# Kernel optimization log

Hardware: AMD Instinct MI355X
Metric: run time of the kernel (lower is better)

The kernel has to match this reference:

```python
import jax, jax.numpy as jnp
import numpy as np

B, T, IMG, P, D, H, L = 4, 32, 84, 14, 768, 12, 3
GP = IMG // P            # 6 patches per side
NP = GP * GP             # 36 patches
N = NP + 1               # +cls token
FF = 4 * D
HD = D // H


def _ln(x, g, b):
    m = jnp.mean(x, -1, keepdims=True)
    v = jnp.var(x, -1, keepdims=True)
    return (x - m) * jax.lax.rsqrt(v + 1e-5) * g + b


def _mha(x, qkv_w, qkv_b, proj_w, proj_b):
    Bn, Nn, C = x.shape
    qkv = (x @ qkv_w + qkv_b).reshape(Bn, Nn, 3, H, HD).transpose(2, 0, 3, 1, 4)
    q, k, v = qkv[0], qkv[1], qkv[2]                      # (B,H,N,hd)
    attn = jax.nn.softmax(jnp.einsum('bhqd,bhkd->bhqk', q, k) * HD ** -0.5, axis=-1)
    o = jnp.einsum('bhqk,bhkd->bhqd', attn, v).transpose(0, 2, 1, 3).reshape(Bn, Nn, C)
    return o @ proj_w + proj_b


def _blocks(x, pre_g, pre_b, n1_g, n1_b, qkv_w, qkv_b, proj_w, proj_b,
            n2_g, n2_b, fc1_w, fc1_b, fc2_w, fc2_b):
    # TemporalViT applies an extra pre-norm, then x = x + Block(x_norm),
    # where Block itself contains two residual sublayers on x_norm.
    for i in range(L):
        xn = _ln(x, pre_g[i], pre_b[i])
        y = xn + _mha(_ln(xn, n1_g[i], n1_b[i]), qkv_w[i], qkv_b[i], proj_w[i], proj_b[i])
        h = jax.nn.gelu(_ln(y, n2_g[i], n2_b[i]) @ fc1_w[i] + fc1_b[i], approximate=False)
        y = y + h @ fc2_w[i] + fc2_b[i]
        x = x + y
    return x


def _forward(x, conv_w, conv_b, cls, pos, tpos,
             s_pre_g, s_pre_b, s_n1_g, s_n1_b, s_qkv_w, s_qkv_b, s_proj_w, s_proj_b,
             s_n2_g, s_n2_b, s_fc1_w, s_fc1_b, s_fc2_w, s_fc2_b,
             t_pre_g, t_pre_b, t_n1_g, t_n1_b, t_qkv_w, t_qkv_b, t_proj_w, t_proj_b,
             t_n2_g, t_n2_b, t_fc1_w, t_fc1_b, t_fc2_w, t_fc2_b):
    xf = x.reshape(B * T, 3, IMG, IMG)
    p = jax.lax.conv_general_dilated(xf, conv_w, (P, P), 'VALID',
                                     dimension_numbers=('NCHW', 'OIHW', 'NCHW'))
    p = p + conv_b[None, :, None, None]                  # (BT, D, 6, 6)
    p = p.reshape(B * T, D, NP).transpose(0, 2, 1)       # (BT, 36, D)
    p = jnp.concatenate([jnp.broadcast_to(cls, (B * T, 1, D)), p], axis=1) + pos
    p = _blocks(p, s_pre_g, s_pre_b, s_n1_g, s_n1_b, s_qkv_w, s_qkv_b, s_proj_w,
                s_proj_b, s_n2_g, s_n2_b, s_fc1_w, s_fc1_b, s_fc2_w, s_fc2_b)
    p = p.reshape(B, T * N, D)
    tp = jnp.broadcast_to(tpos[:, :T, None, :], (1, T, N, D)).reshape(1, T * N, D)
    p = p + tp
    p = _blocks(p, t_pre_g, t_pre_b, t_n1_g, t_n1_b, t_qkv_w, t_qkv_b, t_proj_w,
                t_proj_b, t_n2_g, t_n2_b, t_fc1_w, t_fc1_b, t_fc2_w, t_fc2_b)
    return p.mean(axis=1)                                # (B, D)


def setup_inputs() -> dict:
    key = jax.random.key(0)
    ks = iter(jax.random.split(key, 64))
    r = lambda shape, s=0.02: (jax.random.normal(next(ks), shape, jnp.float32) * s)
    inp = {
        'x': jax.random.normal(next(ks), (B, T, 3, IMG, IMG), jnp.float32),
        'conv_w': r((D, 3, P, P)), 'conv_b': jnp.zeros((D,), jnp.float32),
        'cls': r((1, 1, D)), 'pos': r((1, N, D)), 'tpos': r((1, 100, D)),
    }
    for pfx in ('s', 't'):
        inp[f'{pfx}_pre_g'] = jnp.ones((L, D), jnp.float32)
        inp[f'{pfx}_pre_b'] = jnp.zeros((L, D), jnp.float32)
        inp[f'{pfx}_n1_g'] = jnp.ones((L, D), jnp.float32)
        inp[f'{pfx}_n1_b'] = jnp.zeros((L, D), jnp.float32)
        inp[f'{pfx}_qkv_w'] = r((L, D, 3 * D))
        inp[f'{pfx}_qkv_b'] = jnp.zeros((L, 3 * D), jnp.float32)
        inp[f'{pfx}_proj_w'] = r((L, D, D))
        inp[f'{pfx}_proj_b'] = jnp.zeros((L, D), jnp.float32)
        inp[f'{pfx}_n2_g'] = jnp.ones((L, D), jnp.float32)
        inp[f'{pfx}_n2_b'] = jnp.zeros((L, D), jnp.float32)
        inp[f'{pfx}_fc1_w'] = r((L, D, FF))
        inp[f'{pfx}_fc1_b'] = jnp.zeros((L, FF), jnp.float32)
        inp[f'{pfx}_fc2_w'] = r((L, FF, D))
        inp[f'{pfx}_fc2_b'] = jnp.zeros((L, D), jnp.float32)
    return inp


def reference(x, conv_w, conv_b, cls, pos, tpos,
              s_pre_g, s_pre_b, s_n1_g, s_n1_b, s_qkv_w, s_qkv_b, s_proj_w, s_proj_b,
              s_n2_g, s_n2_b, s_fc1_w, s_fc1_b, s_fc2_w, s_fc2_b,
              t_pre_g, t_pre_b, t_n1_g, t_n1_b, t_qkv_w, t_qkv_b, t_proj_w, t_proj_b,
              t_n2_g, t_n2_b, t_fc1_w, t_fc1_b, t_fc2_w, t_fc2_b):
    return _forward(x, conv_w, conv_b, cls, pos, tpos,
                    s_pre_g, s_pre_b, s_n1_g, s_n1_b, s_qkv_w, s_qkv_b, s_proj_w,
                    s_proj_b, s_n2_g, s_n2_b, s_fc1_w, s_fc1_b, s_fc2_w, s_fc2_b,
                    t_pre_g, t_pre_b, t_n1_g, t_n1_b, t_qkv_w, t_qkv_b, t_proj_w,
                    t_proj_b, t_n2_g, t_n2_b, t_fc1_w, t_fc1_b, t_fc2_w, t_fc2_b)
```

## Files before the change

### kernel.cpp

```cpp
#include <hip/hip_runtime.h>
#include <math.h>

#define NTOK 4736
#define MPAD 4864
#define DM   768
#define NHEAD 12
#define KC   640

typedef __attribute__((ext_vector_type(8))) short bf16x8;
typedef __attribute__((ext_vector_type(4))) float f32x4;

__device__ inline short f2bf(float f) {
  union { float f; unsigned u; } v; v.f = f;
  unsigned r = v.u + 0x7FFF + ((v.u >> 16) & 1);
  return (short)(r >> 16);
}

__device__ inline void gload16(const void* g, void* l) {
  __builtin_amdgcn_global_load_lds(
      (const __attribute__((address_space(1))) void*)g,
      (__attribute__((address_space(3))) void*)l, 16, 0, 0);
}

__global__ __launch_bounds__(256) void im2col_k(const float* __restrict__ x,
                                                short* __restrict__ col) {
  int i = blockIdx.x * 256 + threadIdx.x;
  int r = i / KC, k = i % KC;
  short v = 0;
  if (k < 588) {
    int bt = r / 36, p = r % 36;
    int gy = p / 6, gx = p % 6;
    int c = k / 196, rem = k % 196;
    int ky = rem / 14, kx = rem % 14;
    v = f2bf(x[(((size_t)bt * 3 + c) * 84 + gy * 14 + ky) * 84 + gx * 14 + kx]);
  }
  col[i] = v;
}

__global__ __launch_bounds__(256) void convw_k(const float* __restrict__ w,
                                               short* __restrict__ out) {
  int i = blockIdx.x * 256 + threadIdx.x;
  int n = i / KC, k = i % KC;
  out[i] = (k < 588) ? f2bf(w[(size_t)n * 588 + k]) : (short)0;
}

__global__ __launch_bounds__(256) void wt_k(const float* __restrict__ in,
                                            short* __restrict__ out,
                                            int K, int N) {
  __shared__ float tile[32][33];
  const int l = blockIdx.z;
  in  += (size_t)l * K * N;
  out += (size_t)l * N * K;
  const int n0 = blockIdx.x * 32, k0 = blockIdx.y * 32;
  const int tx = threadIdx.x & 31, ty = threadIdx.x >> 5;
#pragma unroll
  for (int r = 0; r < 4; r++)
    tile[ty + 8 * r][tx] = in[(size_t)(k0 + ty + 8 * r) * N + n0 + tx];
  __syncthreads();
#pragma unroll
  for (int r = 0; r < 4; r++)
    out[(size_t)(n0 + ty + 8 * r) * K + k0 + tx] = f2bf(tile[tx][ty + 8 * r]);
}

__global__ __launch_bounds__(256) void assemble_k(const float* __restrict__ conv_out,
                                                  const float* __restrict__ cls,
                                                  const float* __restrict__ pos,
                                                  float* __restrict__ X) {
  int i = blockIdx.x * 256 + threadIdx.x;
  int t = i / DM, d = i % DM;
  int bt = t / 37, n = t % 37;
  float v = (n == 0) ? cls[d] : conv_out[((size_t)bt * 36 + (n - 1)) * DM + d];
  X[i] = v + pos[n * DM + d];
}

__global__ __launch_bounds__(256) void tpos_k(float* __restrict__ X,
                                              const float* __restrict__ tpos) {
  int i = blockIdx.x * 256 + threadIdx.x;
  int row = i / DM, d = i % DM;
  int tt = (row % 1184) / 37;
  X[i] += tpos[tt * DM + d];
}

template <bool OBF>
__global__ __launch_bounds__(256) void ln_k(const float* __restrict__ in,
                                            const float* __restrict__ g,
                                            const float* __restrict__ b,
                                            void* __restrict__ outp) {
  int r = blockIdx.x;
  int tid = threadIdx.x;
  const float* xr = in + (size_t)r * DM;
  float v0 = xr[tid], v1 = xr[tid + 256], v2 = xr[tid + 512];
  float s  = v0 + v1 + v2;
  float sq = v0 * v0 + v1 * v1 + v2 * v2;
#pragma unroll
  for (int off = 32; off; off >>= 1) {
    s  += __shfl_down(s, off);
    sq += __shfl_down(sq, off);
  }
  __shared__ float ss[4], sg[4];
  if ((tid & 63) == 0) { ss[tid >> 6] = s; sg[tid >> 6] = sq; }
  __syncthreads();
  float S = ss[0] + ss[1] + ss[2] + ss[3];
  float Q = sg[0] + sg[1] + sg[2] + sg[3];
  float mean = S * (1.f / 768.f);
  float var  = Q * (1.f / 768.f) - mean * mean;
  float rs = rsqrtf(var + 1e-5f);
  float o0 = (v0 - mean) * rs * g[tid]       + b[tid];
  float o1 = (v1 - mean) * rs * g[tid + 256] + b[tid + 256];
  float o2 = (v2 - mean) * rs * g[tid + 512] + b[tid + 512];
  if (OBF) {
    short* o = (short*)outp + (size_t)r * DM;
    o[tid] = f2bf(o0); o[tid + 256] = f2bf(o1); o[tid + 512] = f2bf(o2);
  } else {
    float* o = (float*)outp + (size_t)r * DM;
    o[tid] = o0; o[tid + 256] = o1; o[tid + 512] = o2;
  }
}

__global__ __launch_bounds__(256) void ln2_k(const float* __restrict__ in,
                                             const float* __restrict__ g1,
                                             const float* __restrict__ b1,
                                             const float* __restrict__ g2,
                                             const float* __restrict__ b2,
                                             float* __restrict__ xn,
                                             short* __restrict__ w) {
  int r = blockIdx.x;
  int tid = threadIdx.x;
  const float* xr = in + (size_t)r * DM;
  float v0 = xr[tid], v1 = xr[tid + 256], v2 = xr[tid + 512];
  float s  = v0 + v1 + v2;
  float sq = v0 * v0 + v1 * v1 + v2 * v2;
#pragma unroll
  for (int off = 32; off; off >>= 1) {
    s  += __shfl_down(s, off);
    sq += __shfl_down(sq, off);
  }
  __shared__ float ss[4], sg[4], ss2[4], sg2[4];
  if ((tid & 63) == 0) { ss[tid >> 6] = s; sg[tid >> 6] = sq; }
  __syncthreads();
  float S = ss[0] + ss[1] + ss[2] + ss[3];
  float Q = sg[0] + sg[1] + sg[2] + sg[3];
  float mean = S * (1.f / 768.f);
  float var  = Q * (1.f / 768.f) - mean * mean;
  float rs = rsqrtf(var + 1e-5f);
  float x0 = (v0 - mean) * rs * g1[tid]       + b1[tid];
  float x1 = (v1 - mean) * rs * g1[tid + 256] + b1[tid + 256];
  float x2 = (v2 - mean) * rs * g1[tid + 512] + b1[tid + 512];
  float* xo = xn + (size_t)r * DM;
  xo[tid] = x0; xo[tid + 256] = x1; xo[tid + 512] = x2;
  float s2  = x0 + x1 + x2;
  float sq2 = x0 * x0 + x1 * x1 + x2 * x2;
#pragma unroll
  for (int off = 32; off; off >>= 1) {
    s2  += __shfl_down(s2, off);
    sq2 += __shfl_down(sq2, off);
  }
  if ((tid & 63) == 0) { ss2[tid >> 6] = s2; sg2[tid >> 6] = sq2; }
  __syncthreads();
  float S2 = ss2[0] + ss2[1] + ss2[2] + ss2[3];
  float Q2 = sg2[0] + sg2[1] + sg2[2] + sg2[3];
  float mean2 = S2 * (1.f / 768.f);
  float var2  = Q2 * (1.f / 768.f) - mean2 * mean2;
  float rs2 = rsqrtf(var2 + 1e-5f);
  short* wo = w + (size_t)r * DM;
  wo[tid]       = f2bf((x0 - mean2) * rs2 * g2[tid]       + b2[tid]);
  wo[tid + 256] = f2bf((x1 - mean2) * rs2 * g2[tid + 256] + b2[tid + 256]);
  wo[tid + 512] = f2bf((x2 - mean2) * rs2 * g2[tid + 512] + b2[tid + 512]);
}

template <int BM, int BN, int WM, int WN, bool GELU, bool OBF, bool HASR1, bool HASR2>
__global__ __launch_bounds__(256, 2) void tgemm_k(const short* __restrict__ A,
                                                  const short* __restrict__ Bw,
                                                  const float* __restrict__ bias,
                                                  const float* __restrict__ r1,
                                                  const float* __restrict__ r2,
                                                  void* __restrict__ Cout,
                                                  int M, int N, int K) {
  constexpr int TM = BM / WM, TN = BN / WN;
  constexpr int MF = TM / 16, NF = TN / 16;
  constexpr int RPC = 32;
  constexpr int ACH = BM / RPC, BCH = BN / RPC;
  constexpr int LOADS = ACH + BCH;

  __shared__ short As[2][BM][64];
  __shared__ short Bs[2][BN][64];

  const int nwg  = gridDim.x * gridDim.y;
  const int orig = blockIdx.x + gridDim.x * blockIdx.y;
  const int qq = nwg >> 3, rr = nwg & 7;
  const int xcd = orig & 7, sub = orig >> 3;
  const int wgid = ((xcd < rr) ? xcd * (qq + 1) : rr * (qq + 1) + (xcd - rr) * qq) + sub;
  const int gy = gridDim.y;
  const int bm = (wgid / gy) * BM, bn = (wgid % gy) * BN;

  const int tid = threadIdx.x, wid = tid >> 6, lane = tid & 63;
  const int lr = lane & 15, lg = lane >> 4;
  const int wm = wid / WN, wn = wid % WN;

  const int srow = tid >> 3;
  const int sslot = (tid & 7) ^ (srow & 7);
  const short* Asrc = A  + (size_t)(bm + srow) * K + sslot * 8;
  const short* Bsrc = Bw + (size_t)(bn + srow) * K + sslot * 8;

  f32x4 acc[MF][NF];
#pragma unroll
  for (int m = 0; m < MF; m++)
#pragma unroll
    for (int n = 0; n < NF; n++) acc[m][n] = (f32x4){0.f, 0.f, 0.f, 0.f};

#define STAGE(slot, kk)                                                        \
  do {                                                                         \
    _Pragma("unroll")                                                          \
    for (int j = 0; j < ACH; j++)                                              \
      gload16(Asrc + (size_t)(j * RPC) * K + (kk),                             \
              (char*)&As[slot][0][0] + j * RPC * 128 + wid * 1024);            \
    _Pragma("unroll")                                                          \
    for (int j = 0; j < BCH; j++)                                              \
      gload16(Bsrc + (size_t)(j * RPC) * K + (kk),                             \
              (char*)&Bs[slot][0][0] + j * RPC * 128 + wid * 1024);            \
  } while (0)

  const int NT = K >> 6;
  const int swz = (lr & 7) << 4;

  STAGE(0, 0);
  for (int t = 0; t < NT; t++) {
    const int c = t & 1;
    if (t + 1 < NT) STAGE(c ^ 1, (t + 1) << 6);
    if (t + 1 < NT) {
      if constexpr (LOADS == 8)      asm volatile("s_waitcnt vmcnt(8)" ::: "memory");
      else if constexpr (LOADS == 6) asm volatile("s_waitcnt vmcnt(6)" ::: "memory");
      else                           asm volatile("s_waitcnt vmcnt(0)" ::: "memory");
    } else {
      asm volatile("s_waitcnt vmcnt(0)" ::: "memory");
    }
    __builtin_amdgcn_s_barrier();

    bf16x8 bq[NF][2], aq[MF][2];
#pragma unroll
    for (int nf = 0; nf < NF; nf++) {
      const int row = wn * TN + nf * 16 + lr;
#pragma unroll
      for (int ks = 0; ks < 2; ks++)
        bq[nf][ks] = *reinterpret_cast<const bf16x8*>(
            (const char*)&Bs[c][0][0] + row * 128 + ((ks * 64 + lg * 16) ^ swz));
    }
#pragma unroll
    for (int mf = 0; mf < MF; mf++) {
      const int row = wm * TM + mf * 16 + lr;
#pragma unroll
      for (int ks = 0; ks < 2; ks++)
        aq[mf][ks] = *reinterpret_cast<const bf16x8*>(
            (const char*)&As[c][0][0] + row * 128 + ((ks * 64 + lg * 16) ^ swz));
    }
    __builtin_amdgcn_s_setprio(1);
#pragma unroll
    for (int mf = 0; mf < MF; mf++)
#pragma unroll
      for (int nf = 0; nf < NF; nf++) {
        acc[mf][nf] = __builtin_amdgcn_mfma_f32_16x16x32_bf16(
            aq[mf][0], bq[nf][0], acc[mf][nf], 0, 0, 0);
        acc[mf][nf] = __builtin_amdgcn_mfma_f32_16x16x32_bf16(
            aq[mf][1], bq[nf][1], acc[mf][nf], 0, 0, 0);
      }
    __builtin_amdgcn_s_setprio(0);
    __builtin_amdgcn_s_barrier();
  }
#undef STAGE

#pragma unroll
  for (int m = 0; m < MF; m++) {
#pragma unroll
    for (int r = 0; r < 4; r++) {
      int row = bm + wm * TM + m * 16 + lg * 4 + r;
      if (row < M) {
#pragma unroll
        for (int n = 0; n < NF; n++) {
          int col = bn + wn * TN + n * 16 + lr;
          size_t idx = (size_t)row * N + col;
          float v = acc[m][n][r];
          if (bias) v += bias[col];
          if (GELU) v = 0.5f * v * (1.f + erff(v * 0.70710678118654752f));
          if (HASR1) v += r1[idx];
          if (HASR2) v += r2[idx];
          if (OBF) ((short*)Cout)[idx] = f2bf(v);
          else     ((float*)Cout)[idx] = v;
        }
      }
    }
  }
}

__global__ __launch_bounds__(256) void attn_k(const short* __restrict__ qkv,
                                              short* __restrict__ out,
                                              int Bn, int Nn) {
  const int gx = gridDim.x, gy = gridDim.y;
  const int nwg = gx * gy;
  const int orig = blockIdx.x + gx * blockIdx.y;
  const int qq = nwg >> 3, rr = nwg & 7;
  const int xcd = orig & 7, sub = orig >> 3;
  const int wgid = ((xcd < rr) ? xcd * (qq + 1) : rr * (qq + 1) + (xcd - rr) * qq) + sub;
  const int bh = wgid / gy;
  const int qb = wgid % gy;
  const int b = bh / NHEAD, h = bh % NHEAD;
  const int q0 = qb * 64;

  const int tid = threadIdx.x;
  const int wid = tid >> 6, lane = tid & 63;
  const int lr = lane & 15, lg = lane >> 4;

  __shared__ short Ks[64][64];
  __shared__ short Vt[64][64];
  __shared__ short Ps[4][16][64];

  const int qrow_in = q0 + wid * 16 + lr;
  const int qcl = (qrow_in < Nn) ? qrow_in : (Nn - 1);
  const short* qp = qkv + ((size_t)(b * Nn + qcl)) * 2304 + h * 64 + lg * 8;
  bf16x8 qa0 = *reinterpret_cast<const bf16x8*>(qp);
  bf16x8 qa1 = *reinterpret_cast<const bf16x8*>(qp + 32);

  f32x4 oo[4];
#pragma unroll
  for (int dg = 0; dg < 4; dg++) oo[dg] = (f32x4){0.f, 0.f, 0.f, 0.f};
  float mm[4] = {-1e30f, -1e30f, -1e30f, -1e30f};
  float ll[4] = {0.f, 0.f, 0.f, 0.f};

  const int skey = tid >> 2;
  const int sdq  = (tid & 3) * 16;
  const int vkey = tid & 63;
  const int vd0  = wid * 16;

  const int swr = (lr & 7) << 3;

  for (int k0 = 0; k0 < Nn; k0 += 64) {
    {
      int kg = k0 + skey; if (kg >= Nn) kg = Nn - 1;
      const short* kp = qkv + ((size_t)(b * Nn + kg)) * 2304 + 768 + h * 64 + sdq;
      bf16x8 ka = *reinterpret_cast<const bf16x8*>(kp);
      bf16x8 kb = *reinterpret_cast<const bf16x8*>(kp + 8);
      const int ksw = (skey & 7) << 3;
      *reinterpret_cast<bf16x8*>(&Ks[skey][sdq ^ ksw])       = ka;
      *reinterpret_cast<bf16x8*>(&Ks[skey][(sdq + 8) ^ ksw]) = kb;
      int vg = k0 + vkey; if (vg >= Nn) vg = Nn - 1;
      const short* vp = qkv + ((size_t)(b * Nn + vg)) * 2304 + 1536 + h * 64 + vd0;
      bf16x8 va = *reinterpret_cast<const bf16x8*>(vp);
      bf16x8 vb = *reinterpret_cast<const bf16x8*>(vp + 8);
#pragma unroll
      for (int i = 0; i < 8; i++) {
        Vt[vd0 + i][vkey ^ (i << 3)]     = va[i];
        Vt[vd0 + 8 + i][vkey ^ (i << 3)] = vb[i];
      }
    }
    __syncthreads();

    f32x4 c[4];
#pragma unroll
    for (int kf = 0; kf < 4; kf++) {
      c[kf] = (f32x4){0.f, 0.f, 0.f, 0.f};
      const short* krow = &Ks[kf * 16 + lr][0];
      bf16x8 kb0 = *reinterpret_cast<const bf16x8*>(krow + ((lg * 8) ^ swr));
      c[kf] = __builtin_amdgcn_mfma_f32_16x16x32_bf16(qa0, kb0, c[kf], 0, 0, 0);
      bf16x8 kb1 = *reinterpret_cast<const bf16x8*>(krow + ((32 + lg * 8) ^ swr));
      c[kf] = __builtin_amdgcn_mfma_f32_16x16x32_bf16(qa1, kb1, c[kf], 0, 0, 0);
    }
#pragma unroll
    for (int kf = 0; kf < 4; kf++) {
#pragma unroll
      for (int r = 0; r < 4; r++) c[kf][r] *= 0.125f;
      if (k0 + kf * 16 + lr >= Nn)
        c[kf][0] = c[kf][1] = c[kf][2] = c[kf][3] = -1e30f;
    }

#pragma unroll
    for (int r = 0; r < 4; r++) {
      float t = fmaxf(fmaxf(c[0][r], c[1][r]), fmaxf(c[2][r], c[3][r]));
      t = fmaxf(t, __shfl_xor(t, 1, 16));
      t = fmaxf(t, __shfl_xor(t, 2, 16));
      t = fmaxf(t, __shfl_xor(t, 4, 16));
      t = fmaxf(t, __shfl_xor(t, 8, 16));
      float mn = fmaxf(mm[r], t);
      float sc = __expf(mm[r] - mn);
      float p0 = __expf(c[0][r] - mn);
      float p1 = __expf(c[1][r] - mn);
      float p2 = __expf(c[2][r] - mn);
      float p3 = __expf(c[3][r] - mn);
      float ps = (p0 + p1) + (p2 + p3);
      ps += __shfl_xor(ps, 1, 16);
      ps += __shfl_xor(ps, 2, 16);
      ps += __shfl_xor(ps, 4, 16);
      ps += __shfl_xor(ps, 8, 16);
      ll[r] = ll[r] * sc + ps;
      mm[r] = mn;
      oo[0][r] *= sc; oo[1][r] *= sc; oo[2][r] *= sc; oo[3][r] *= sc;
      const int prow = lg * 4 + r;
      const int psw  = (prow & 7) << 3;
      short* pr = &Ps[wid][prow][0];
      pr[lr ^ psw]        = f2bf(p0);
      pr[(16 + lr) ^ psw] = f2bf(p1);
      pr[(32 + lr) ^ psw] = f2bf(p2);
      pr[(48 + lr) ^ psw] = f2bf(p3);
    }

#pragma unroll
    for (int ks = 0; ks < 2; ks++) {
      bf16x8 pa = *reinterpret_cast<const bf16x8*>(&Ps[wid][lr][(ks * 32 + lg * 8) ^ swr]);
#pragma unroll
      for (int dg = 0; dg < 4; dg++) {
        bf16x8 vb = *reinterpret_cast<const bf16x8*>(
            &Vt[dg * 16 + lr][(ks * 32 + lg * 8) ^ swr]);
        oo[dg] = __builtin_amdgcn_mfma_f32_16x16x32_bf16(pa, vb, oo[dg], 0, 0, 0);
      }
    }
    __syncthreads();
  }

#pragma unroll
  for (int r = 0; r < 4; r++) {
    int qr = q0 + wid * 16 + lg * 4 + r;
    if (qr < Nn) {
      float inv = 1.f / ll[r];
      short* op = out + ((size_t)(b * Nn + qr)) * DM + h * 64 + lr;
      op[0]  = f2bf(oo[0][r] * inv);
      op[16] = f2bf(oo[1][r] * inv);
      op[32] = f2bf(oo[2][r] * inv);
      op[48] = f2bf(oo[3][r] * inv);
    }
  }
}

__global__ __launch_bounds__(256) void mean1_k(const float* __restrict__ X,
                                               float* __restrict__ P) {
  int b = blockIdx.x, seg = blockIdx.z;
  int d = blockIdx.y * 256 + threadIdx.x;
  int r0 = seg * 148;
  float s = 0.f;
  for (int r = r0; r < r0 + 148; r++) s += X[((size_t)b * 1184 + r) * DM + d];
  P[((size_t)(b * 8 + seg)) * DM + d] = s;
}
__global__ __launch_bounds__(256) void mean2_k(const float* __restrict__ P,
                                               float* __restrict__ out) {
  int b = blockIdx.x;
  int d = blockIdx.y * 256 + threadIdx.x;
  float s = 0.f;
#pragma unroll
  for (int seg = 0; seg < 8; seg++) s += P[((size_t)(b * 8 + seg)) * DM + d];
  out[b * DM + d] = s * (1.f / 1184.f);
}

extern "C" void kernel_launch(void* const* d_in, const int* in_sizes, int n_in,
                              void* d_out, int out_size, void* d_ws, size_t ws_size,
                              hipStream_t stream) {
  (void)in_sizes; (void)n_in; (void)out_size; (void)ws_size;
  const float* x      = (const float*)d_in[0];
  const float* conv_w = (const float*)d_in[1];
  const float* conv_b = (const float*)d_in[2];
  const float* cls    = (const float*)d_in[3];
  const float* pos    = (const float*)d_in[4];
  const float* tpos   = (const float*)d_in[5];
  const float* W[2][14];
  for (int p = 0; p < 2; p++)
    for (int i = 0; i < 14; i++)
      W[p][i] = (const float*)d_in[6 + p * 14 + i];

  char* ws = (char*)d_ws;
  const size_t TOKF = (size_t)NTOK * DM * 4;
  float* X    = (float*)(ws);
  float* XN   = (float*)(ws + TOKF);
  float* Y    = (float*)(ws + 2 * TOKF);
  short* TA2  = (short*)(ws + 3 * TOKF);
  short* BIG  = (short*)(ws + 3 * TOKF + (size_t)MPAD * DM * 2);
  short* WB   = (short*)(ws + 3 * TOKF + (size_t)MPAD * DM * 2
                            + (size_t)MPAD * 3072 * 2);
  const size_t QE = (size_t)3 * 2304 * 768;
  const size_t PE = (size_t)3 * 768 * 768;
  const size_t F1E = (size_t)3 * 3072 * 768;
  const size_t F2E = (size_t)3 * 768 * 3072;
  const size_t PFX = QE + PE + F1E + F2E;
  short* WQ[2], *WP[2], *WF1[2], *WF2[2];
  for (int p = 0; p < 2; p++) {
    WQ[p]  = WB + p * PFX;
    WP[p]  = WQ[p] + QE;
    WF1[p] = WP[p] + PE;
    WF2[p] = WF1[p] + F1E;
  }
  short* CW = WB + 2 * PFX;
  float* PB = (float*)(CW + (size_t)768 * KC);

  for (int p = 0; p < 2; p++) {
    wt_k<<<dim3(72, 24, 3), 256, 0, stream>>>(W[p][4],  WQ[p],  768, 2304);
    wt_k<<<dim3(24, 24, 3), 256, 0, stream>>>(W[p][6],  WP[p],  768, 768);
    wt_k<<<dim3(96, 24, 3), 256, 0, stream>>>(W[p][10], WF1[p], 768, 3072);
    wt_k<<<dim3(24, 96, 3), 256, 0, stream>>>(W[p][12], WF2[p], 3072, 768);
  }
  convw_k<<<1920, 256, 0, stream>>>(conv_w, CW);

  im2col_k<<<11520, 256, 0, stream>>>(x, BIG);
  tgemm_k<64, 128, 1, 4, false, false, false, false><<<dim3(72, 6), 256, 0, stream>>>(
      BIG, CW, conv_b, nullptr, nullptr, Y, 4608, 768, KC);
  assemble_k<<<14208, 256, 0, stream>>>(Y, cls, pos, X);

  for (int phase = 0; phase < 2; phase++) {
    const int Bn = (phase == 0) ? 128 : 4;
    const int Nn = (phase == 0) ? 37 : 1184;
    if (phase == 1) tpos_k<<<14208, 256, 0, stream>>>(X, tpos);
    for (int i = 0; i < 3; i++) {
      const float* pre_g = W[phase][0] + i * DM;
      const float* pre_b = W[phase][1] + i * DM;
      const float* n1_g  = W[phase][2] + i * DM;
      const float* n1_b  = W[phase][3] + i * DM;
      const float* qkv_b = W[phase][5] + i * 2304;
      const float* prj_b = W[phase][7] + i * DM;
      const float* n2_g  = W[phase][8] + i * DM;
      const float* n2_b  = W[phase][9] + i * DM;
      const float* fc1_b = W[phase][11] + i * 3072;
      const float* fc2_b = W[phase][13] + i * DM;
      const short* qkv_w = WQ[phase]  + (size_t)i * 2304 * 768;
      const short* prj_w = WP[phase]  + (size_t)i * 768 * 768;
      const short* fc1_w = WF1[phase] + (size_t)i * 3072 * 768;
      const short* fc2_w = WF2[phase] + (size_t)i * 768 * 3072;

      ln2_k<<<NTOK, 256, 0, stream>>>(X, pre_g, pre_b, n1_g, n1_b, XN, TA2);
      tgemm_k<128, 128, 2, 2, false, true, false, false><<<dim3(37, 18), 256, 0, stream>>>(
          TA2, qkv_w, qkv_b, nullptr, nullptr, BIG, NTOK, 2304, DM);
      attn_k<<<dim3(Bn * NHEAD, (Nn + 63) / 64), 256, 0, stream>>>(BIG, TA2, Bn, Nn);
      tgemm_k<64, 128, 1, 4, false, false, true, false><<<dim3(74, 6), 256, 0, stream>>>(
          TA2, prj_w, prj_b, XN, nullptr, Y, NTOK, DM, DM);
      ln_k<true><<<NTOK, 256, 0, stream>>>(Y, n2_g, n2_b, TA2);
      tgemm_k<128, 128, 2, 2, true, true, false, false><<<dim3(37, 24), 256, 0, stream>>>(
          TA2, fc1_w, fc1_b, nullptr, nullptr, BIG, NTOK, 3072, DM);
      tgemm_k<64, 128, 1, 4, false, false, true, true><<<dim3(74, 6), 256, 0, stream>>>(
          BIG, fc2_w, fc2_b, Y, X, X, NTOK, DM, 3072);
    }
  }
  mean1_k<<<dim3(4, 3, 8), 256, 0, stream>>>(X, PB);
  mean2_k<<<dim3(4, 3), 256, 0, stream>>>(PB, (float*)d_out);
}
```

Before: 1.612 ms.

## Replace LDS-staged GEMM with register-direct global-load MFMA GEMM

Replaces the double-buffered LDS-staged GEMM with a kernel in which each wave loads its A and B fragments straight from global memory into registers and feeds the MFMAs, with no shared memory or barriers. This is meant to remove LDS traffic and synchronisation overhead. In exchange there is no cross-wave reuse through LDS, so every wave refetches its operands from L2. The global reads are also strided 16-byte loads without software pipelining, and the padded-M buffers and the row bound check are dropped.

```diff
diff --git a/kernel.cpp b/kernel.cpp
--- a/kernel.cpp
+++ b/kernel.cpp
@@ -2,7 +2,6 @@
 #include <math.h>
 
 #define NTOK 4736
-#define MPAD 4864
 #define DM   768
 #define NHEAD 12
 #define KC   640
@@ -14,12 +13,6 @@
   union { float f; unsigned u; } v; v.f = f;
   unsigned r = v.u + 0x7FFF + ((v.u >> 16) & 1);
   return (short)(r >> 16);
-}
-
-__device__ inline void gload16(const void* g, void* l) {
-  __builtin_amdgcn_global_load_lds(
-      (const __attribute__((address_space(1))) void*)g,
-      (__attribute__((address_space(3))) void*)l, 16, 0, 0);
 }
 
 __global__ __launch_bounds__(256) void im2col_k(const float* __restrict__ x,
@@ -168,124 +161,76 @@
   wo[tid + 512] = f2bf((x2 - mean2) * rs2 * g2[tid + 512] + b2[tid + 512]);
 }
 
-template <int BM, int BN, int WM, int WN, bool GELU, bool OBF, bool HASR1, bool HASR2>
-__global__ __launch_bounds__(256, 2) void tgemm_k(const short* __restrict__ A,
-                                                  const short* __restrict__ Bw,
-                                                  const float* __restrict__ bias,
-                                                  const float* __restrict__ r1,
-                                                  const float* __restrict__ r2,
-                                                  void* __restrict__ Cout,
-                                                  int M, int N, int K) {
-  constexpr int TM = BM / WM, TN = BN / WN;
-  constexpr int MF = TM / 16, NF = TN / 16;
-  constexpr int RPC = 32;
-  constexpr int ACH = BM / RPC, BCH = BN / RPC;
-  constexpr int LOADS = ACH + BCH;
-
-  __shared__ short As[2][BM][64];
-  __shared__ short Bs[2][BN][64];
-
+template <int WM, int WN, bool GELU, bool OBF, bool HASR1, bool HASR2>
+__global__ __launch_bounds__(WM * WN * 64) void rgemm_k(const short* __restrict__ A,
+                                                        const short* __restrict__ Bw,
+                                                        const float* __restrict__ bias,
+                                                        const float* __restrict__ r1,
+                                                        const float* __restrict__ r2,
+                                                        void* __restrict__ Cout,
+                                                        int M, int N, int K) {
   const int nwg  = gridDim.x * gridDim.y;
   const int orig = blockIdx.x + gridDim.x * blockIdx.y;
   const int qq = nwg >> 3, rr = nwg & 7;
   const int xcd = orig & 7, sub = orig >> 3;
   const int wgid = ((xcd < rr) ? xcd * (qq + 1) : rr * (qq + 1) + (xcd - rr) * qq) + sub;
   const int gy = gridDim.y;
-  const int bm = (wgid / gy) * BM, bn = (wgid % gy) * BN;
+  const int bm = (wgid / gy) * (WM * 64), bn = (wgid % gy) * (WN * 64);
 
   const int tid = threadIdx.x, wid = tid >> 6, lane = tid & 63;
   const int lr = lane & 15, lg = lane >> 4;
   const int wm = wid / WN, wn = wid % WN;
 
-  const int srow = tid >> 3;
-  const int sslot = (tid & 7) ^ (srow & 7);
-  const short* Asrc = A  + (size_t)(bm + srow) * K + sslot * 8;
-  const short* Bsrc = Bw + (size_t)(bn + srow) * K + sslot * 8;
-
-  f32x4 acc[MF][NF];
-#pragma unroll
-  for (int m = 0; m < MF; m++)
-#pragma unroll
-    for (int n = 0; n < NF; n++) acc[m][n] = (f32x4){0.f, 0.f, 0.f, 0.f};
-
-#define STAGE(slot, kk)                                                        \
-  do {                                                                         \
-    _Pragma("unroll")                                                          \
-    for (int j = 0; j < ACH; j++)                                              \
-      gload16(Asrc + (size_t)(j * RPC) * K + (kk),                             \
-              (char*)&As[slot][0][0] + j * RPC * 128 + wid * 1024);            \
-    _Pragma("unroll")                                                          \
-    for (int j = 0; j < BCH; j++)                                              \
-      gload16(Bsrc + (size_t)(j * RPC) * K + (kk),                             \
-              (char*)&Bs[slot][0][0] + j * RPC * 128 + wid * 1024);            \
-  } while (0)
-
-  const int NT = K >> 6;
-  const int swz = (lr & 7) << 4;
-
-  STAGE(0, 0);
-  for (int t = 0; t < NT; t++) {
-    const int c = t & 1;
-    if (t + 1 < NT) STAGE(c ^ 1, (t + 1) << 6);
-    if (t + 1 < NT) {
-      if constexpr (LOADS == 8)      asm volatile("s_waitcnt vmcnt(8)" ::: "memory");
-      else if constexpr (LOADS == 6) asm volatile("s_waitcnt vmcnt(6)" ::: "memory");
-      else                           asm volatile("s_waitcnt vmcnt(0)" ::: "memory");
-    } else {
-      asm volatile("s_waitcnt vmcnt(0)" ::: "memory");
-    }
-    __builtin_amdgcn_s_barrier();
-
-    bf16x8 bq[NF][2], aq[MF][2];
-#pragma unroll
-    for (int nf = 0; nf < NF; nf++) {
-      const int row = wn * TN + nf * 16 + lr;
+  const short* Ap0 = A  + (size_t)(bm + wm * 64 + lr) * K + lg * 8;
+  const short* Bp0 = Bw + (size_t)(bn + wn * 64 + lr) * K + lg * 8;
+
+  f32x4 acc[4][4];
+#pragma unroll
+  for (int m = 0; m < 4; m++)
+#pragma unroll
+    for (int n = 0; n < 4; n++) acc[m][n] = (f32x4){0.f, 0.f, 0.f, 0.f};
+
+  for (int k0 = 0; k0 < K; k0 += 64) {
+    bf16x8 aq[4][2], bq[4][2];
+#pragma unroll
+    for (int mf = 0; mf < 4; mf++)
+#pragma unroll
+      for (int ks = 0; ks < 2; ks++)
+        aq[mf][ks] = *reinterpret_cast<const bf16x8*>(
+            Ap0 + (size_t)(mf * 16) * K + k0 + ks * 32);
+#pragma unroll
+    for (int nf = 0; nf < 4; nf++)
 #pragma unroll
       for (int ks = 0; ks < 2; ks++)
         bq[nf][ks] = *reinterpret_cast<const bf16x8*>(
-            (const char*)&Bs[c][0][0] + row * 128 + ((ks * 64 + lg * 16) ^ swz));
-    }
-#pragma unroll
-    for (int mf = 0; mf < MF; mf++) {
-      const int row = wm * TM + mf * 16 + lr;
-#pragma unroll
-      for (int ks = 0; ks < 2; ks++)
-        aq[mf][ks] = *reinterpret_cast<const bf16x8*>(
-            (const char*)&As[c][0][0] + row * 128 + ((ks * 64 + lg * 16) ^ swz));
-    }
-    __builtin_amdgcn_s_setprio(1);
-#pragma unroll
-    for (int mf = 0; mf < MF; mf++)
-#pragma unroll
-      for (int nf = 0; nf < NF; nf++) {
+            Bp0 + (size_t)(nf * 16) * K + k0 + ks * 32);
+#pragma unroll
+    for (int mf = 0; mf < 4; mf++)
+#pragma unroll
+      for (int nf = 0; nf < 4; nf++) {
         acc[mf][nf] = __builtin_amdgcn_mfma_f32_16x16x32_bf16(
             aq[mf][0], bq[nf][0], acc[mf][nf], 0, 0, 0);
         acc[mf][nf] = __builtin_amdgcn_mfma_f32_16x16x32_bf16(
             aq[mf][1], bq[nf][1], acc[mf][nf], 0, 0, 0);
       }
-    __builtin_amdgcn_s_setprio(0);
-    __builtin_amdgcn_s_barrier();
-  }
-#undef STAGE
-
-#pragma unroll
-  for (int m = 0; m < MF; m++) {
+  }
+
+#pragma unroll
+  for (int m = 0; m < 4; m++) {
 #pragma unroll
     for (int r = 0; r < 4; r++) {
-      int row = bm + wm * TM + m * 16 + lg * 4 + r;
-      if (row < M) {
-#pragma unroll
-        for (int n = 0; n < NF; n++) {
-          int col = bn + wn * TN + n * 16 + lr;
-          size_t idx = (size_t)row * N + col;
-          float v = acc[m][n][r];
-          if (bias) v += bias[col];
-          if (GELU) v = 0.5f * v * (1.f + erff(v * 0.70710678118654752f));
-          if (HASR1) v += r1[idx];
-          if (HASR2) v += r2[idx];
-          if (OBF) ((short*)Cout)[idx] = f2bf(v);
-          else     ((float*)Cout)[idx] = v;
-        }
+      int row = bm + wm * 64 + m * 16 + lg * 4 + r;
+#pragma unroll
+      for (int n = 0; n < 4; n++) {
+        int col = bn + wn * 64 + n * 16 + lr;
+        size_t idx = (size_t)row * N + col;
+        float v = acc[m][n][r];
+        if (bias) v += bias[col];
+        if (GELU) v = 0.5f * v * (1.f + erff(v * 0.70710678118654752f));
+        if (HASR1) v += r1[idx];
+        if (HASR2) v += r2[idx];
+        if (OBF) ((short*)Cout)[idx] = f2bf(v);
+        else     ((float*)Cout)[idx] = v;
       }
     }
   }
@@ -468,9 +413,9 @@
   float* XN   = (float*)(ws + TOKF);
   float* Y    = (float*)(ws + 2 * TOKF);
   short* TA2  = (short*)(ws + 3 * TOKF);
-  short* BIG  = (short*)(ws + 3 * TOKF + (size_t)MPAD * DM * 2);
-  short* WB   = (short*)(ws + 3 * TOKF + (size_t)MPAD * DM * 2
-                            + (size_t)MPAD * 3072 * 2);
+  short* BIG  = (short*)(ws + 3 * TOKF + (size_t)NTOK * DM * 2);
+  short* WB   = (short*)(ws + 3 * TOKF + (size_t)NTOK * DM * 2
+                            + (size_t)NTOK * 3072 * 2);
   const size_t QE = (size_t)3 * 2304 * 768;
   const size_t PE = (size_t)3 * 768 * 768;
   const size_t F1E = (size_t)3 * 3072 * 768;
@@ -495,7 +440,7 @@
   convw_k<<<1920, 256, 0, stream>>>(conv_w, CW);
 
   im2col_k<<<11520, 256, 0, stream>>>(x, BIG);
-  tgemm_k<64, 128, 1, 4, false, false, false, false><<<dim3(72, 6), 256, 0, stream>>>(
+  rgemm_k<2, 1, false, false, false, false><<<dim3(36, 12), 128, 0, stream>>>(
       BIG, CW, conv_b, nullptr, nullptr, Y, 4608, 768, KC);
   assemble_k<<<14208, 256, 0, stream>>>(Y, cls, pos, X);
 
@@ -520,15 +465,15 @@
       const short* fc2_w = WF2[phase] + (size_t)i * 768 * 3072;
 
       ln2_k<<<NTOK, 256, 0, stream>>>(X, pre_g, pre_b, n1_g, n1_b, XN, TA2);
-      tgemm_k<128, 128, 2, 2, false, true, false, false><<<dim3(37, 18), 256, 0, stream>>>(
+      rgemm_k<2, 2, false, true, false, false><<<dim3(37, 18), 256, 0, stream>>>(
           TA2, qkv_w, qkv_b, nullptr, nullptr, BIG, NTOK, 2304, DM);
       attn_k<<<dim3(Bn * NHEAD, (Nn + 63) / 64), 256, 0, stream>>>(BIG, TA2, Bn, Nn);
-      tgemm_k<64, 128, 1, 4, false, false, true, false><<<dim3(74, 6), 256, 0, stream>>>(
+      rgemm_k<2, 1, false, false, true, false><<<dim3(37, 12), 128, 0, stream>>>(
           TA2, prj_w, prj_b, XN, nullptr, Y, NTOK, DM, DM);
       ln_k<true><<<NTOK, 256, 0, stream>>>(Y, n2_g, n2_b, TA2);
-      tgemm_k<128, 128, 2, 2, true, true, false, false><<<dim3(37, 24), 256, 0, stream>>>(
+      rgemm_k<2, 2, true, true, false, false><<<dim3(37, 24), 256, 0, stream>>>(
           TA2, fc1_w, fc1_b, nullptr, nullptr, BIG, NTOK, 3072, DM);
-      tgemm_k<64, 128, 1, 4, false, false, true, true><<<dim3(74, 6), 256, 0, stream>>>(
+      rgemm_k<2, 1, false, false, true, true><<<dim3(37, 12), 128, 0, stream>>>(
           BIG, fc2_w, fc2_b, Y, X, X, NTOK, DM, 3072);
     }
   }
```

New measurement: 2.929 ms. 1.82x slower.
